# Kernel optimization log

Measured on AMD Instinct MI355X. Metric: run time of the kernel, lower is better.

The kernel has to match this reference:

```python
import jax, jax.numpy as jnp
import numpy as np

N = 100000   # nodes
B = 64       # graphs in batch
E = 1600000  # edges
D_IN = 2
W1D = W2D = W3D = 128
N_CLASSES = 3
MIN_SCORE = 0.1
TOL = 1e-7
BN_EPS = 1e-5


def setup_inputs() -> dict:
    key = jax.random.key(0)
    ks = jax.random.split(key, 32)
    inp = {}
    inp['x'] = jax.random.normal(ks[0], (N, D_IN), jnp.float32)
    inp['edge_index'] = jax.random.randint(ks[1], (2, E), 0, N, dtype=jnp.int32)
    inp['batch_index'] = jnp.sort(jax.random.randint(ks[2], (N,), 0, B, dtype=jnp.int32))
    inp['topk_w'] = jax.random.normal(ks[3], (D_IN,), jnp.float32)
    dims = [(D_IN, W1D), (W1D, W2D), (W2D, W3D)]
    k = 4
    for i, (din, dout) in enumerate(dims, start=1):
        inp[f'W{i}'] = jax.random.normal(ks[k], (din, dout), jnp.float32) * (1.0 / np.sqrt(din)); k += 1
        inp[f'b{i}'] = jax.random.normal(ks[k], (dout,), jnp.float32) * 0.05; k += 1
        inp[f'g{i}'] = 1.0 + 0.1 * jax.random.normal(ks[k], (dout,), jnp.float32); k += 1
        inp[f'be{i}'] = 0.1 * jax.random.normal(ks[k], (dout,), jnp.float32); k += 1
        inp[f'rm{i}'] = 0.1 * jax.random.normal(ks[k], (dout,), jnp.float32); k += 1
        inp[f'rv{i}'] = 1.0 + 0.1 * jax.random.uniform(ks[k], (dout,), jnp.float32); k += 1
    inp['linW'] = jax.random.normal(ks[k], (W3D, N_CLASSES), jnp.float32) * (1.0 / np.sqrt(W3D)); k += 1
    inp['linb'] = jax.random.normal(ks[k], (N_CLASSES,), jnp.float32) * 0.05
    return inp


def _bn_eval(x, g, be, rm, rv):
    # BatchNorm1d in eval mode (running stats)
    return (x - rm) * jax.lax.rsqrt(rv + BN_EPS) * g + be


def _gcn(x, src, dst, ew, W, b):
    # GCNConv: lin -> symmetric-normalized scatter-add (self-loops already in src/dst/ew)
    xw = x @ W                                   # [N, dout]
    deg = jax.ops.segment_sum(ew, dst, num_segments=N)
    dinv = jnp.where(deg > 0, jax.lax.rsqrt(deg), 0.0)
    norm = dinv[src] * ew * dinv[dst]            # [E+N]
    out = jax.ops.segment_sum(norm[:, None] * xw[src], dst, num_segments=N)
    return out + b


def reference(x, edge_index, batch_index, topk_w,
              W1, b1, g1, be1, rm1, rv1,
              W2, b2, g2, be2, rm2, rv2,
              W3, b3, g3, be3, rm3, rv3,
              linW, linb):
    # ---- TopKPooling (min_score mode): per-graph softmax score, threshold keep,
    # x scaled by score. Implemented via masking (fixed shapes): dropped nodes get
    # zero features, zero edge weights, and -inf at the max pool -> math identical
    # to PyG's node filtering (BN is eval-mode, i.e. per-node).
    logits = x @ topk_w                                                    # [N]
    m = jax.ops.segment_max(logits, batch_index, num_segments=B)
    e = jnp.exp(logits - m[batch_index])
    score = e / jax.ops.segment_sum(e, batch_index, num_segments=B)[batch_index]
    smax = jax.ops.segment_max(score, batch_index, num_segments=B)[batch_index] - TOL
    keep = score > jnp.minimum(smax, MIN_SCORE)                            # [N] bool
    keep_f = keep.astype(x.dtype)
    h = x * (score * keep_f)[:, None]

    src0, dst0 = edge_index[0], edge_index[1]
    loop = jnp.arange(N, dtype=src0.dtype)
    src = jnp.concatenate([src0, loop])
    dst = jnp.concatenate([dst0, loop])
    ew = jnp.concatenate([keep_f[src0] * keep_f[dst0], keep_f])            # mask + self-loops

    h = _bn_eval(jax.nn.relu(_gcn(h, src, dst, ew, W1, b1)), g1, be1, rm1, rv1)
    h = _bn_eval(jax.nn.relu(_gcn(h, src, dst, ew, W2, b2)), g2, be2, rm2, rv2)
    h = _bn_eval(jax.nn.relu(_gcn(h, src, dst, ew, W3, b3)), g3, be3, rm3, rv3)

    neg = jnp.finfo(h.dtype).min
    h = jnp.where(keep[:, None], h, neg)
    pooled = jax.ops.segment_max(h, batch_index, num_segments=B)           # [B, w3]
    out = pooled @ linW + linb
    return jax.nn.log_softmax(out, axis=1)
```

## Files before the change

kernel.cpp:

```cpp
#include <hip/hip_runtime.h>

#define NN 100000
#define BB 64
#define EE 1600000
#define FD 128
#define SLOTC 64
#define KSLOTS (BB * SLOTC)
#define EMAXE (1 << 20)
#define NWORDS (NN / 32)
#define STR 391

__device__ __forceinline__ int plower(const int* __restrict__ bidx, int v,
                                      int tid, int* ired) {
    int p = tid * STR;
    int val = bidx[p];
    ired[tid] = (val < v) ? tid : -1;
    __syncthreads();
    for (int s = 128; s > 0; s >>= 1) { if (tid < s) ired[tid] = max(ired[tid], ired[tid + s]); __syncthreads(); }
    int t0 = ired[0];
    __syncthreads();
    if (t0 < 0) return 0;
    int lo = t0 * STR;
    int hi = lo + STR; if (hi > NN) hi = NN;
    int ans = hi;
    for (int q = lo + 1 + tid; q < hi; q += 256) {
        if (bidx[q] >= v) { ans = q; break; }
    }
    ired[tid] = ans;
    __syncthreads();
    for (int s = 128; s > 0; s >>= 1) { if (tid < s) ired[tid] = min(ired[tid], ired[tid + s]); __syncthreads(); }
    int r = ired[0];
    __syncthreads();
    return r;
}

__global__ __launch_bounds__(256) void k_scorekeep(
    const float2* __restrict__ x, const int* __restrict__ bidx,
    const float* __restrict__ tw,
    unsigned* __restrict__ kfbits, int* __restrict__ nslot,
    int* __restrict__ knt, float* __restrict__ degs, float2* __restrict__ h0s,
    int* __restrict__ kecnt)
{
    __shared__ int   ired[256];
    __shared__ float red[256];
    __shared__ int   klist[SLOTC];
    __shared__ int   lcnt;
    __shared__ float shv;
    int b = blockIdx.x, tid = threadIdx.x;
    if (tid == 0) { lcnt = 0; if (b == 0) { kecnt[0] = 0; kecnt[1] = 0; } }
    int s0 = plower(bidx, b, tid, ired);
    int e0 = plower(bidx, b + 1, tid, ired);
    int L = e0 - s0;
    float w0 = tw[0], w1 = tw[1];

    if (L > 0) {
        int wlo = s0 >> 5, whi = (e0 - 1) >> 5;
        for (int w = wlo + tid; w <= whi; w += 256) {
            unsigned mask = 0xFFFFFFFFu;
            if (w == wlo) mask &= (0xFFFFFFFFu << (s0 & 31));
            if (w == whi) mask &= (0xFFFFFFFFu >> (31 - ((e0 - 1) & 31)));
            if (mask == 0xFFFFFFFFu) kfbits[w] = 0u;
            else atomicAnd(&kfbits[w], ~mask);
        }
    }

    float mx = -3.4028235e38f;
    for (int j = tid; j < L; j += 256) {
        float2 v = x[s0 + j];
        mx = fmaxf(mx, v.x * w0 + v.y * w1);
    }
    red[tid] = mx; __syncthreads();
    for (int s = 128; s > 0; s >>= 1) { if (tid < s) red[tid] = fmaxf(red[tid], red[tid + s]); __syncthreads(); }
    if (tid == 0) shv = red[0];
    __syncthreads();
    float m = shv;

    float sm = 0.f;
    for (int j = tid; j < L; j += 256) {
        float2 v = x[s0 + j];
        sm += expf(v.x * w0 + v.y * w1 - m);
    }
    red[tid] = sm; __syncthreads();
    for (int s = 128; s > 0; s >>= 1) { if (tid < s) red[tid] += red[tid + s]; __syncthreads(); }
    if (tid == 0) shv = red[0];
    __syncthreads();
    float S = shv;
    float thr = fminf(1.0f / S - 1e-7f, 0.1f);

    for (int j = tid; j < L; j += 256) {
        float2 v = x[s0 + j];
        float sc = expf(v.x * w0 + v.y * w1 - m) / S;
        if (sc > thr) {
            int l = atomicAdd(&lcnt, 1);
            if (l < SLOTC) klist[l] = j;
        }
    }
    __syncthreads();
    int nk = lcnt; if (nk > SLOTC) nk = SLOTC;
    if (tid == 0) knt[b] = nk;
    for (int l = tid; l < nk; l += 256) {
        int i = s0 + klist[l];
        float2 v = x[i];
        float sc = expf(v.x * w0 + v.y * w1 - m) / S;
        int slot = b * SLOTC + l;
        atomicOr(&kfbits[i >> 5], 1u << (i & 31));
        nslot[i] = slot;
        degs[slot] = 1.0f;
        h0s[slot] = make_float2(v.x * sc, v.y * sc);
    }
}

__global__ void k_edges(const int4* __restrict__ src4, const int* __restrict__ ei,
                        const unsigned* __restrict__ kfbits, const int* __restrict__ nslot,
                        float* __restrict__ degs, int* __restrict__ kedge,
                        int* __restrict__ kecnt) {
    int t = blockIdx.x * 256 + threadIdx.x;
    if (t * 4 >= EE) return;
    int4 s4 = src4[t];
    int ss[4] = {s4.x, s4.y, s4.z, s4.w};
    #pragma unroll
    for (int q = 0; q < 4; q++) {
        int s = ss[q];
        if ((kfbits[s >> 5] >> (s & 31)) & 1u) {
            int d = ei[EE + t * 4 + q];
            if ((kfbits[d >> 5] >> (d & 31)) & 1u) {
                int ds = nslot[d], sl = nslot[s];
                atomicAdd(&degs[ds], 1.0f);
                int idx = atomicAdd(&kecnt[0], 1);
                if (idx < EMAXE) { kedge[2 * idx] = sl; kedge[2 * idx + 1] = ds; }
                if ((sl >> 6) != (ds >> 6)) atomicAdd(&kecnt[1], 1);
            }
        }
    }
}

__global__ __launch_bounds__(256) void k_tail_main(
    const float* __restrict__ degs, const float2* __restrict__ h0s,
    const int* __restrict__ kedge, const int* __restrict__ kecnt,
    const int* __restrict__ knt,
    const float* __restrict__ W1, const float* __restrict__ b1,
    const float* __restrict__ g1, const float* __restrict__ be1,
    const float* __restrict__ rm1, const float* __restrict__ rv1,
    const float* __restrict__ W2, const float* __restrict__ b2,
    const float* __restrict__ g2, const float* __restrict__ be2,
    const float* __restrict__ rm2, const float* __restrict__ rv2,
    const float* __restrict__ W3, const float* __restrict__ b3,
    const float* __restrict__ g3, const float* __restrict__ be3,
    const float* __restrict__ rm3, const float* __restrict__ rv3,
    const float* __restrict__ linW, const float* __restrict__ linb,
    float* __restrict__ hY, float* __restrict__ out)
{
    __shared__ float tileA[SLOTC * FD];
    __shared__ float tileB[SLOTC * FD];
    __shared__ float2 psl[SLOTC];
    __shared__ float poolv[FD];
    __shared__ int keS;
    int b = blockIdx.x, tid = threadIdx.x;
    if (tid == 0) { int k = kecnt[0]; keS = k > EMAXE ? EMAXE : k; }
    for (int j = tid; j < SLOTC; j += 256) psl[j] = make_float2(0.f, 0.f);
    __syncthreads();
    int ke = keS, nk = knt[b], cross = kecnt[1];

    for (int t = tid; t < ke; t += 256) {
        int d = kedge[2 * t + 1];
        if ((d >> 6) == b) {
            int s = kedge[2 * t];
            float nm = rsqrtf(degs[s]) * rsqrtf(degs[d]);
            float2 h = h0s[s];
            atomicAdd(&psl[d & 63].x, nm * h.x);
            atomicAdd(&psl[d & 63].y, nm * h.y);
        }
    }
    __syncthreads();
    for (int j = tid; j < nk * FD; j += 256) {
        int ld = j >> 7, f = j & 127, slot = b * SLOTC + ld;
        float di = rsqrtf(degs[slot]), d2 = di * di;
        float2 h = h0s[slot];
        float a0 = psl[ld].x + d2 * h.x;
        float a1 = psl[ld].y + d2 * h.y;
        float v = a0 * W1[f] + a1 * W1[FD + f] + b1[f];
        v = fmaxf(v, 0.f);
        v = (v - rm1[f]) * rsqrtf(rv1[f] + 1e-5f) * g1[f] + be1[f];
        tileA[j] = v;
    }
    __syncthreads();
    for (int j = tid; j < nk * FD; j += 256) {
        int ld = j >> 7, f = j & 127;
        const float* xr = tileA + ld * FD;
        float acc = 0.f;
        #pragma unroll 8
        for (int k = 0; k < FD; k++) acc += xr[k] * W2[k * FD + f];
        tileB[j] = acc;
    }
    __syncthreads();
    if (cross != 0) {
        for (int j = tid; j < nk * FD; j += 256) {
            int ld = j >> 7, f = j & 127;
            hY[(b * SLOTC + ld) * FD + f] = tileB[j];
        }
        return;
    }
    for (int j = tid; j < nk * FD; j += 256) tileA[j] = 0.f;
    __syncthreads();
    for (long long idx = tid; idx < (long long)ke * FD; idx += 256) {
        int e = (int)(idx >> 7), f = (int)(idx & 127);
        int d = kedge[2 * e + 1];
        if ((d >> 6) == b) {
            int s = kedge[2 * e];
            float nm = rsqrtf(degs[s]) * rsqrtf(degs[d]);
            atomicAdd(&tileA[(d & 63) * FD + f], nm * tileB[(s & 63) * FD + f]);
        }
    }
    __syncthreads();
    for (int j = tid; j < nk * FD; j += 256) {
        int ld = j >> 7, f = j & 127, slot = b * SLOTC + ld;
        float di = rsqrtf(degs[slot]);
        float v = tileA[j] + di * di * tileB[j] + b2[f];
        v = fmaxf(v, 0.f);
        v = (v - rm2[f]) * rsqrtf(rv2[f] + 1e-5f) * g2[f] + be2[f];
        tileA[j] = v;
    }
    __syncthreads();
    for (int j = tid; j < nk * FD; j += 256) {
        int ld = j >> 7, f = j & 127;
        const float* xr = tileA + ld * FD;
        float acc = 0.f;
        #pragma unroll 8
        for (int k = 0; k < FD; k++) acc += xr[k] * W3[k * FD + f];
        tileB[j] = acc;
    }
    __syncthreads();
    for (int j = tid; j < nk * FD; j += 256) tileA[j] = 0.f;
    __syncthreads();
    for (long long idx = tid; idx < (long long)ke * FD; idx += 256) {
        int e = (int)(idx >> 7), f = (int)(idx & 127);
        int d = kedge[2 * e + 1];
        if ((d >> 6) == b) {
            int s = kedge[2 * e];
            float nm = rsqrtf(degs[s]) * rsqrtf(degs[d]);
            atomicAdd(&tileA[(d & 63) * FD + f], nm * tileB[(s & 63) * FD + f]);
        }
    }
    __syncthreads();
    for (int j = tid; j < nk * FD; j += 256) {
        int ld = j >> 7, f = j & 127, slot = b * SLOTC + ld;
        float di = rsqrtf(degs[slot]);
        float v = tileA[j] + di * di * tileB[j] + b3[f];
        v = fmaxf(v, 0.f);
        v = (v - rm3[f]) * rsqrtf(rv3[f] + 1e-5f) * g3[f] + be3[f];
        tileA[j] = v;
    }
    __syncthreads();
    for (int f = tid; f < FD; f += 256) {
        float mx = -3.4028235e38f;
        for (int ld = 0; ld < nk; ld++) mx = fmaxf(mx, tileA[ld * FD + f]);
        poolv[f] = mx;
    }
    __syncthreads();
    if (tid == 0) {
        float z0 = linb[0], z1 = linb[1], z2 = linb[2];
        for (int f = 0; f < FD; f++) {
            float pv = poolv[f];
            z0 += pv * linW[f * 3 + 0];
            z1 += pv * linW[f * 3 + 1];
            z2 += pv * linW[f * 3 + 2];
        }
        float m = fmaxf(z0, fmaxf(z1, z2));
        float l = m + logf(expf(z0 - m) + expf(z1 - m) + expf(z2 - m));
        out[b * 3 + 0] = z0 - l;
        out[b * 3 + 1] = z1 - l;
        out[b * 3 + 2] = z2 - l;
    }
}

__global__ __launch_bounds__(256) void k_tail_slow(
    const float* __restrict__ degs, const int* __restrict__ kedge,
    const int* __restrict__ kecnt, const int* __restrict__ knt,
    const float* __restrict__ hY,
    const float* __restrict__ b2, const float* __restrict__ g2,
    const float* __restrict__ be2, const float* __restrict__ rm2,
    const float* __restrict__ rv2,
    const float* __restrict__ W3, const float* __restrict__ b3,
    const float* __restrict__ g3, const float* __restrict__ be3,
    const float* __restrict__ rm3, const float* __restrict__ rv3,
    const float* __restrict__ linW, const float* __restrict__ linb,
    float* __restrict__ out)
{
    if (kecnt[1] == 0) return;
    __shared__ float tileA[SLOTC * FD];
    __shared__ float tileB[SLOTC * FD];
    __shared__ float rowt[FD];
    __shared__ float poolv[FD];
    __shared__ int keS;
    int b = blockIdx.x, tid = threadIdx.x;
    if (tid == 0) { int k = kecnt[0]; keS = k > EMAXE ? EMAXE : k; }
    __syncthreads();
    int ke = keS, nk = knt[b];

    for (int j = tid; j < nk * FD; j += 256) tileA[j] = 0.f;
    __syncthreads();
    for (long long idx = tid; idx < (long long)ke * FD; idx += 256) {
        int e = (int)(idx >> 7), f = (int)(idx & 127);
        int d = kedge[2 * e + 1];
        if ((d >> 6) == b) {
            int s = kedge[2 * e];
            float nm = rsqrtf(degs[s]) * rsqrtf(degs[d]);
            atomicAdd(&tileA[(d & 63) * FD + f], nm * hY[s * FD + f]);
        }
    }
    __syncthreads();
    for (int j = tid; j < nk * FD; j += 256) {
        int ld = j >> 7, f = j & 127, slot = b * SLOTC + ld;
        float di = rsqrtf(degs[slot]);
        float v = tileA[j] + di * di * hY[slot * FD + f] + b2[f];
        v = fmaxf(v, 0.f);
        v = (v - rm2[f]) * rsqrtf(rv2[f] + 1e-5f) * g2[f] + be2[f];
        tileA[j] = v;
    }
    __syncthreads();
    for (int j = tid; j < nk * FD; j += 256) {
        int ld = j >> 7, f = j & 127;
        const float* xr = tileA + ld * FD;
        float acc = 0.f;
        #pragma unroll 8
        for (int k = 0; k < FD; k++) acc += xr[k] * W3[k * FD + f];
        tileB[j] = acc;
    }
    __syncthreads();
    for (int j = tid; j < nk * FD; j += 256) tileA[j] = 0.f;
    __syncthreads();
    for (long long idx = tid; idx < (long long)ke * FD; idx += 256) {
        int e = (int)(idx >> 7), f = (int)(idx & 127);
        int d = kedge[2 * e + 1];
        if ((d >> 6) == b) {
            int s = kedge[2 * e];
            if ((s >> 6) == b) {
                float nm = rsqrtf(degs[s]) * rsqrtf(degs[d]);
                atomicAdd(&tileA[(d & 63) * FD + f], nm * tileB[(s & 63) * FD + f]);
            }
        }
    }
    __syncthreads();
    for (int e = 0; e < ke; e++) {
        int d = kedge[2 * e + 1];
        if ((d >> 6) != b) continue;
        int s = kedge[2 * e];
        if ((s >> 6) == b) continue;
        float dis = rsqrtf(degs[s]);
        for (int f = tid; f < FD; f += 256) {
            float acc = dis * dis * hY[s * FD + f];
            for (int e2 = 0; e2 < ke; e2++) {
                if (kedge[2 * e2 + 1] == s) {
                    int u = kedge[2 * e2];
                    acc += rsqrtf(degs[u]) * dis * hY[u * FD + f];
                }
            }
            float v = acc + b2[f];
            v = fmaxf(v, 0.f);
            v = (v - rm2[f]) * rsqrtf(rv2[f] + 1e-5f) * g2[f] + be2[f];
            rowt[f] = v;
        }
        __syncthreads();
        float nm = dis * rsqrtf(degs[d]);
        for (int f = tid; f < FD; f += 256) {
            float acc = 0.f;
            #pragma unroll 8
            for (int k = 0; k < FD; k++) acc += rowt[k] * W3[k * FD + f];
            atomicAdd(&tileA[(d & 63) * FD + f], nm * acc);
        }
        __syncthreads();
    }
    for (int j = tid; j < nk * FD; j += 256) {
        int ld = j >> 7, f = j & 127, slot = b * SLOTC + ld;
        float di = rsqrtf(degs[slot]);
        float v = tileA[j] + di * di * tileB[j] + b3[f];
        v = fmaxf(v, 0.f);
        v = (v - rm3[f]) * rsqrtf(rv3[f] + 1e-5f) * g3[f] + be3[f];
        tileA[j] = v;
    }
    __syncthreads();
    for (int f = tid; f < FD; f += 256) {
        float mx = -3.4028235e38f;
        for (int ld = 0; ld < nk; ld++) mx = fmaxf(mx, tileA[ld * FD + f]);
        poolv[f] = mx;
    }
    __syncthreads();
    if (tid == 0) {
        float z0 = linb[0], z1 = linb[1], z2 = linb[2];
        for (int f = 0; f < FD; f++) {
            float pv = poolv[f];
            z0 += pv * linW[f * 3 + 0];
            z1 += pv * linW[f * 3 + 1];
            z2 += pv * linW[f * 3 + 2];
        }
        float m = fmaxf(z0, fmaxf(z1, z2));
        float l = m + logf(expf(z0 - m) + expf(z1 - m) + expf(z2 - m));
        out[b * 3 + 0] = z0 - l;
        out[b * 3 + 1] = z1 - l;
        out[b * 3 + 2] = z2 - l;
    }
}

extern "C" void kernel_launch(void* const* d_in, const int* in_sizes, int n_in,
                              void* d_out, int out_size, void* d_ws, size_t ws_size,
                              hipStream_t stream) {
    (void)in_sizes; (void)n_in; (void)out_size; (void)ws_size;
    const float* x    = (const float*)d_in[0];
    const int*   ei   = (const int*)d_in[1];
    const int*   bidx = (const int*)d_in[2];
    const float* tw   = (const float*)d_in[3];
    const float* W1 = (const float*)d_in[4],  *b1 = (const float*)d_in[5],  *g1 = (const float*)d_in[6];
    const float* be1= (const float*)d_in[7],  *rm1= (const float*)d_in[8],  *rv1= (const float*)d_in[9];
    const float* W2 = (const float*)d_in[10], *b2 = (const float*)d_in[11], *g2 = (const float*)d_in[12];
    const float* be2= (const float*)d_in[13], *rm2= (const float*)d_in[14], *rv2= (const float*)d_in[15];
    const float* W3 = (const float*)d_in[16], *b3 = (const float*)d_in[17], *g3 = (const float*)d_in[18];
    const float* be3= (const float*)d_in[19], *rm3= (const float*)d_in[20], *rv3= (const float*)d_in[21];
    const float* linW = (const float*)d_in[22], *linb = (const float*)d_in[23];
    float* out = (float*)d_out;

    char* w = (char*)d_ws;
    auto take = [&](size_t bytes) { char* r = w; w += (bytes + 255) & ~(size_t)255; return r; };
    int*      kecnt  = (int*)take(16);
    int*      knt    = (int*)take((size_t)BB * 4);
    unsigned* kfbits = (unsigned*)take((size_t)NWORDS * 4);
    int*      nslot  = (int*)take((size_t)NN * 4);
    float*    degs   = (float*)take((size_t)KSLOTS * 4);
    float2*   h0s    = (float2*)take((size_t)KSLOTS * 8);
    int*      kedge  = (int*)take((size_t)EMAXE * 8);
    float*    hY     = (float*)take((size_t)KSLOTS * FD * 4);

    k_scorekeep<<<BB, 256, 0, stream>>>((const float2*)x, bidx, tw,
                                        kfbits, nslot, knt, degs, h0s, kecnt);
    k_edges<<<(EE / 4 + 255) / 256, 256, 0, stream>>>((const int4*)ei, ei, kfbits,
                                                      nslot, degs, kedge, kecnt);
    k_tail_main<<<BB, 256, 0, stream>>>(degs, h0s, kedge, kecnt, knt,
                                        W1, b1, g1, be1, rm1, rv1,
                                        W2, b2, g2, be2, rm2, rv2,
                                        W3, b3, g3, be3, rm3, rv3,
                                        linW, linb, hY, out);
    k_tail_slow<<<BB, 256, 0, stream>>>(degs, kedge, kecnt, knt, hY,
                                        b2, g2, be2, rm2, rv2,
                                        W3, b3, g3, be3, rm3, rv3,
                                        linW, linb, out);
}
```

Before: 143.2 us.

## Fuse edge filtering and GCN tail into one kernel with last-block finisher

Merges the edge-compaction kernel and both tail kernels into a single grid-strided kernel of 512 blocks. A global atomic counter elects the last-finishing block, which then runs all three GCN layers, pooling and the classifier for every graph, using global scratch buffers instead of per-graph shared tiles. This removes two kernel launches and the slow cross-graph fallback path, but all tail work now runs on a single block, which serialises work that was spread across 64 blocks.

```diff
diff --git a/kernel.cpp b/kernel.cpp
--- a/kernel.cpp
+++ b/kernel.cpp
@@ -9,6 +9,7 @@
 #define EMAXE (1 << 20)
 #define NWORDS (NN / 32)
 #define STR 391
+#define GRIDB 512
 
 __device__ __forceinline__ int plower(const int* __restrict__ bidx, int v,
                                       int tid, int* ired) {
@@ -47,7 +48,7 @@
     __shared__ int   lcnt;
     __shared__ float shv;
     int b = blockIdx.x, tid = threadIdx.x;
-    if (tid == 0) { lcnt = 0; if (b == 0) { kecnt[0] = 0; kecnt[1] = 0; } }
+    if (tid == 0) { lcnt = 0; if (b == 0) { kecnt[0] = 0; kecnt[2] = 0; } }
     int s0 = plower(bidx, b, tid, ired);
     int e0 = plower(bidx, b + 1, tid, ired);
     int L = e0 - s0;
@@ -110,34 +111,11 @@
     }
 }
 
-__global__ void k_edges(const int4* __restrict__ src4, const int* __restrict__ ei,
-                        const unsigned* __restrict__ kfbits, const int* __restrict__ nslot,
-                        float* __restrict__ degs, int* __restrict__ kedge,
-                        int* __restrict__ kecnt) {
-    int t = blockIdx.x * 256 + threadIdx.x;
-    if (t * 4 >= EE) return;
-    int4 s4 = src4[t];
-    int ss[4] = {s4.x, s4.y, s4.z, s4.w};
-    #pragma unroll
-    for (int q = 0; q < 4; q++) {
-        int s = ss[q];
-        if ((kfbits[s >> 5] >> (s & 31)) & 1u) {
-            int d = ei[EE + t * 4 + q];
-            if ((kfbits[d >> 5] >> (d & 31)) & 1u) {
-                int ds = nslot[d], sl = nslot[s];
-                atomicAdd(&degs[ds], 1.0f);
-                int idx = atomicAdd(&kecnt[0], 1);
-                if (idx < EMAXE) { kedge[2 * idx] = sl; kedge[2 * idx + 1] = ds; }
-                if ((sl >> 6) != (ds >> 6)) atomicAdd(&kecnt[1], 1);
-            }
-        }
-    }
-}
-
-__global__ __launch_bounds__(256) void k_tail_main(
-    const float* __restrict__ degs, const float2* __restrict__ h0s,
-    const int* __restrict__ kedge, const int* __restrict__ kecnt,
-    const int* __restrict__ knt,
+__global__ __launch_bounds__(256) void k_edge_tail(
+    const int4* __restrict__ src4, const int* __restrict__ ei,
+    const unsigned* __restrict__ kfbits, const int* __restrict__ nslot,
+    float* __restrict__ degs, int* __restrict__ kedge, int* __restrict__ kecnt,
+    const int* __restrict__ knt, const float2* __restrict__ h0s,
     const float* __restrict__ W1, const float* __restrict__ b1,
     const float* __restrict__ g1, const float* __restrict__ be1,
     const float* __restrict__ rm1, const float* __restrict__ rv1,
@@ -148,247 +126,158 @@
     const float* __restrict__ g3, const float* __restrict__ be3,
     const float* __restrict__ rm3, const float* __restrict__ rv3,
     const float* __restrict__ linW, const float* __restrict__ linb,
-    float* __restrict__ hY, float* __restrict__ out)
+    float* __restrict__ hY, float* __restrict__ hAcc,
+    float* __restrict__ out)
 {
-    __shared__ float tileA[SLOTC * FD];
-    __shared__ float tileB[SLOTC * FD];
-    __shared__ float2 psl[SLOTC];
-    __shared__ float poolv[FD];
-    __shared__ int keS;
-    int b = blockIdx.x, tid = threadIdx.x;
-    if (tid == 0) { int k = kecnt[0]; keS = k > EMAXE ? EMAXE : k; }
-    for (int j = tid; j < SLOTC; j += 256) psl[j] = make_float2(0.f, 0.f);
-    __syncthreads();
-    int ke = keS, nk = knt[b], cross = kecnt[1];
-
+    __shared__ float bufA[SLOTC * FD];
+    __shared__ int   rows[KSLOTS];
+    __shared__ int   knt_s[BB];
+    __shared__ int   offs[BB + 1];
+    __shared__ int   lastFlag;
+    int tid = threadIdx.x;
+
+    const int M = EE / 4;
+    for (int t = blockIdx.x * 256 + tid; t < M; t += GRIDB * 256) {
+        int4 s4 = src4[t];
+        int ss[4] = {s4.x, s4.y, s4.z, s4.w};
+        #pragma unroll
+        for (int q = 0; q < 4; q++) {
+            int s = ss[q];
+            if ((kfbits[s >> 5] >> (s & 31)) & 1u) {
+                int d = ei[EE + t * 4 + q];
+                if ((kfbits[d >> 5] >> (d & 31)) & 1u) {
+                    int ds = nslot[d], sl = nslot[s];
+                    atomicAdd(&degs[ds], 1.0f);
+                    int idx = atomicAdd(&kecnt[0], 1);
+                    if (idx < EMAXE) { kedge[2 * idx] = sl; kedge[2 * idx + 1] = ds; }
+                }
+            }
+        }
+    }
+
+    __threadfence();
+    __syncthreads();
+    if (tid == 0) lastFlag = (atomicAdd(&kecnt[2], 1) == GRIDB - 1);
+    __syncthreads();
+    if (!lastFlag) return;
+    __threadfence();
+
+    int ke = kecnt[0]; if (ke > EMAXE) ke = EMAXE;
+
+    if (tid < BB) knt_s[tid] = knt[tid];
+    __syncthreads();
+    if (tid == 0) {
+        int acc = 0;
+        for (int b = 0; b < BB; b++) { offs[b] = acc; acc += knt_s[b]; }
+        offs[BB] = acc;
+    }
+    __syncthreads();
+    int Rtot = offs[BB];
+    for (int b = tid; b < BB; b += 256)
+        for (int l = 0; l < knt_s[b]; l++) rows[offs[b] + l] = b * SLOTC + l;
+    __syncthreads();
+    int RT = Rtot * FD;
+
+    float2* acc2 = (float2*)bufA;
+    for (int r = tid; r < Rtot; r += 256) acc2[rows[r]] = make_float2(0.f, 0.f);
+    __syncthreads();
     for (int t = tid; t < ke; t += 256) {
-        int d = kedge[2 * t + 1];
-        if ((d >> 6) == b) {
-            int s = kedge[2 * t];
-            float nm = rsqrtf(degs[s]) * rsqrtf(degs[d]);
-            float2 h = h0s[s];
-            atomicAdd(&psl[d & 63].x, nm * h.x);
-            atomicAdd(&psl[d & 63].y, nm * h.y);
-        }
-    }
-    __syncthreads();
-    for (int j = tid; j < nk * FD; j += 256) {
-        int ld = j >> 7, f = j & 127, slot = b * SLOTC + ld;
+        int s = kedge[2 * t], d = kedge[2 * t + 1];
+        float nm = rsqrtf(degs[s]) * rsqrtf(degs[d]);
+        float2 h = h0s[s];
+        atomicAdd(&acc2[d].x, nm * h.x);
+        atomicAdd(&acc2[d].y, nm * h.y);
+    }
+    __syncthreads();
+
+    for (int j = tid; j < RT; j += 256) {
+        int r = j >> 7, f = j & 127, slot = rows[r];
         float di = rsqrtf(degs[slot]), d2 = di * di;
         float2 h = h0s[slot];
-        float a0 = psl[ld].x + d2 * h.x;
-        float a1 = psl[ld].y + d2 * h.y;
+        float a0 = acc2[slot].x + d2 * h.x;
+        float a1 = acc2[slot].y + d2 * h.y;
         float v = a0 * W1[f] + a1 * W1[FD + f] + b1[f];
         v = fmaxf(v, 0.f);
         v = (v - rm1[f]) * rsqrtf(rv1[f] + 1e-5f) * g1[f] + be1[f];
-        tileA[j] = v;
-    }
-    __syncthreads();
-    for (int j = tid; j < nk * FD; j += 256) {
-        int ld = j >> 7, f = j & 127;
-        const float* xr = tileA + ld * FD;
+        hAcc[slot * FD + f] = v;
+    }
+    __syncthreads();
+
+    for (int j = tid; j < RT; j += 256) {
+        int r = j >> 7, f = j & 127, slot = rows[r];
+        const float* xr = hAcc + slot * FD;
         float acc = 0.f;
         #pragma unroll 8
         for (int k = 0; k < FD; k++) acc += xr[k] * W2[k * FD + f];
-        tileB[j] = acc;
-    }
-    __syncthreads();
-    if (cross != 0) {
-        for (int j = tid; j < nk * FD; j += 256) {
-            int ld = j >> 7, f = j & 127;
-            hY[(b * SLOTC + ld) * FD + f] = tileB[j];
-        }
-        return;
-    }
-    for (int j = tid; j < nk * FD; j += 256) tileA[j] = 0.f;
+        hY[slot * FD + f] = acc;
+    }
+    __syncthreads();
+
+    for (int j = tid; j < RT; j += 256) hAcc[rows[j >> 7] * FD + (j & 127)] = 0.f;
     __syncthreads();
     for (long long idx = tid; idx < (long long)ke * FD; idx += 256) {
         int e = (int)(idx >> 7), f = (int)(idx & 127);
-        int d = kedge[2 * e + 1];
-        if ((d >> 6) == b) {
-            int s = kedge[2 * e];
-            float nm = rsqrtf(degs[s]) * rsqrtf(degs[d]);
-            atomicAdd(&tileA[(d & 63) * FD + f], nm * tileB[(s & 63) * FD + f]);
-        }
-    }
-    __syncthreads();
-    for (int j = tid; j < nk * FD; j += 256) {
-        int ld = j >> 7, f = j & 127, slot = b * SLOTC + ld;
+        int s = kedge[2 * e], d = kedge[2 * e + 1];
+        float nm = rsqrtf(degs[s]) * rsqrtf(degs[d]);
+        atomicAdd(&hAcc[d * FD + f], nm * hY[s * FD + f]);
+    }
+    __syncthreads();
+
+    for (int j = tid; j < RT; j += 256) {
+        int r = j >> 7, f = j & 127, slot = rows[r];
         float di = rsqrtf(degs[slot]);
-        float v = tileA[j] + di * di * tileB[j] + b2[f];
+        float v = hAcc[slot * FD + f] + di * di * hY[slot * FD + f] + b2[f];
         v = fmaxf(v, 0.f);
         v = (v - rm2[f]) * rsqrtf(rv2[f] + 1e-5f) * g2[f] + be2[f];
-        tileA[j] = v;
-    }
-    __syncthreads();
-    for (int j = tid; j < nk * FD; j += 256) {
-        int ld = j >> 7, f = j & 127;
-        const float* xr = tileA + ld * FD;
+        hAcc[slot * FD + f] = v;
+    }
+    __syncthreads();
+
+    for (int j = tid; j < RT; j += 256) {
+        int r = j >> 7, f = j & 127, slot = rows[r];
+        const float* xr = hAcc + slot * FD;
         float acc = 0.f;
         #pragma unroll 8
         for (int k = 0; k < FD; k++) acc += xr[k] * W3[k * FD + f];
-        tileB[j] = acc;
-    }
-    __syncthreads();
-    for (int j = tid; j < nk * FD; j += 256) tileA[j] = 0.f;
+        hY[slot * FD + f] = acc;
+    }
+    __syncthreads();
+
+    for (int j = tid; j < RT; j += 256) hAcc[rows[j >> 7] * FD + (j & 127)] = 0.f;
     __syncthreads();
     for (long long idx = tid; idx < (long long)ke * FD; idx += 256) {
         int e = (int)(idx >> 7), f = (int)(idx & 127);
-        int d = kedge[2 * e + 1];
-        if ((d >> 6) == b) {
-            int s = kedge[2 * e];
-            float nm = rsqrtf(degs[s]) * rsqrtf(degs[d]);
-            atomicAdd(&tileA[(d & 63) * FD + f], nm * tileB[(s & 63) * FD + f]);
-        }
-    }
-    __syncthreads();
-    for (int j = tid; j < nk * FD; j += 256) {
-        int ld = j >> 7, f = j & 127, slot = b * SLOTC + ld;
+        int s = kedge[2 * e], d = kedge[2 * e + 1];
+        float nm = rsqrtf(degs[s]) * rsqrtf(degs[d]);
+        atomicAdd(&hAcc[d * FD + f], nm * hY[s * FD + f]);
+    }
+    __syncthreads();
+
+    for (int j = tid; j < RT; j += 256) {
+        int r = j >> 7, f = j & 127, slot = rows[r];
         float di = rsqrtf(degs[slot]);
-        float v = tileA[j] + di * di * tileB[j] + b3[f];
+        float v = hAcc[slot * FD + f] + di * di * hY[slot * FD + f] + b3[f];
         v = fmaxf(v, 0.f);
         v = (v - rm3[f]) * rsqrtf(rv3[f] + 1e-5f) * g3[f] + be3[f];
-        tileA[j] = v;
-    }
-    __syncthreads();
-    for (int f = tid; f < FD; f += 256) {
+        hAcc[slot * FD + f] = v;
+    }
+    __syncthreads();
+
+    float* pool = bufA;
+    for (int j = tid; j < BB * FD; j += 256) {
+        int b = j >> 7, f = j & 127;
         float mx = -3.4028235e38f;
-        for (int ld = 0; ld < nk; ld++) mx = fmaxf(mx, tileA[ld * FD + f]);
-        poolv[f] = mx;
-    }
-    __syncthreads();
-    if (tid == 0) {
+        int nk = knt_s[b];
+        for (int l = 0; l < nk; l++) mx = fmaxf(mx, hAcc[(b * SLOTC + l) * FD + f]);
+        pool[j] = mx;
+    }
+    __syncthreads();
+
+    if (tid < BB) {
+        int b = tid;
         float z0 = linb[0], z1 = linb[1], z2 = linb[2];
         for (int f = 0; f < FD; f++) {
-            float pv = poolv[f];
-            z0 += pv * linW[f * 3 + 0];
-            z1 += pv * linW[f * 3 + 1];
-            z2 += pv * linW[f * 3 + 2];
-        }
-        float m = fmaxf(z0, fmaxf(z1, z2));
-        float l = m + logf(expf(z0 - m) + expf(z1 - m) + expf(z2 - m));
-        out[b * 3 + 0] = z0 - l;
-        out[b * 3 + 1] = z1 - l;
-        out[b * 3 + 2] = z2 - l;
-    }
-}
-
-__global__ __launch_bounds__(256) void k_tail_slow(
-    const float* __restrict__ degs, const int* __restrict__ kedge,
-    const int* __restrict__ kecnt, const int* __restrict__ knt,
-    const float* __restrict__ hY,
-    const float* __restrict__ b2, const float* __restrict__ g2,
-    const float* __restrict__ be2, const float* __restrict__ rm2,
-    const float* __restrict__ rv2,
-    const float* __restrict__ W3, const float* __restrict__ b3,
-    const float* __restrict__ g3, const float* __restrict__ be3,
-    const float* __restrict__ rm3, const float* __restrict__ rv3,
-    const float* __restrict__ linW, const float* __restrict__ linb,
-    float* __restrict__ out)
-{
-    if (kecnt[1] == 0) return;
-    __shared__ float tileA[SLOTC * FD];
-    __shared__ float tileB[SLOTC * FD];
-    __shared__ float rowt[FD];
-    __shared__ float poolv[FD];
-    __shared__ int keS;
-    int b = blockIdx.x, tid = threadIdx.x;
-    if (tid == 0) { int k = kecnt[0]; keS = k > EMAXE ? EMAXE : k; }
-    __syncthreads();
-    int ke = keS, nk = knt[b];
-
-    for (int j = tid; j < nk * FD; j += 256) tileA[j] = 0.f;
-    __syncthreads();
-    for (long long idx = tid; idx < (long long)ke * FD; idx += 256) {
-        int e = (int)(idx >> 7), f = (int)(idx & 127);
-        int d = kedge[2 * e + 1];
-        if ((d >> 6) == b) {
-            int s = kedge[2 * e];
-            float nm = rsqrtf(degs[s]) * rsqrtf(degs[d]);
-            atomicAdd(&tileA[(d & 63) * FD + f], nm * hY[s * FD + f]);
-        }
-    }
-    __syncthreads();
-    for (int j = tid; j < nk * FD; j += 256) {
-        int ld = j >> 7, f = j & 127, slot = b * SLOTC + ld;
-        float di = rsqrtf(degs[slot]);
-        float v = tileA[j] + di * di * hY[slot * FD + f] + b2[f];
-        v = fmaxf(v, 0.f);
-        v = (v - rm2[f]) * rsqrtf(rv2[f] + 1e-5f) * g2[f] + be2[f];
-        tileA[j] = v;
-    }
-    __syncthreads();
-    for (int j = tid; j < nk * FD; j += 256) {
-        int ld = j >> 7, f = j & 127;
-        const float* xr = tileA + ld * FD;
-        float acc = 0.f;
-        #pragma unroll 8
-        for (int k = 0; k < FD; k++) acc += xr[k] * W3[k * FD + f];
-        tileB[j] = acc;
-    }
-    __syncthreads();
-    for (int j = tid; j < nk * FD; j += 256) tileA[j] = 0.f;
-    __syncthreads();
-    for (long long idx = tid; idx < (long long)ke * FD; idx += 256) {
-        int e = (int)(idx >> 7), f = (int)(idx & 127);
-        int d = kedge[2 * e + 1];
-        if ((d >> 6) == b) {
-            int s = kedge[2 * e];
-            if ((s >> 6) == b) {
-                float nm = rsqrtf(degs[s]) * rsqrtf(degs[d]);
-                atomicAdd(&tileA[(d & 63) * FD + f], nm * tileB[(s & 63) * FD + f]);
-            }
-        }
-    }
-    __syncthreads();
-    for (int e = 0; e < ke; e++) {
-        int d = kedge[2 * e + 1];
-        if ((d >> 6) != b) continue;
-        int s = kedge[2 * e];
-        if ((s >> 6) == b) continue;
-        float dis = rsqrtf(degs[s]);
-        for (int f = tid; f < FD; f += 256) {
-            float acc = dis * dis * hY[s * FD + f];
-            for (int e2 = 0; e2 < ke; e2++) {
-                if (kedge[2 * e2 + 1] == s) {
-                    int u = kedge[2 * e2];
-                    acc += rsqrtf(degs[u]) * dis * hY[u * FD + f];
-                }
-            }
-            float v = acc + b2[f];
-            v = fmaxf(v, 0.f);
-            v = (v - rm2[f]) * rsqrtf(rv2[f] + 1e-5f) * g2[f] + be2[f];
-            rowt[f] = v;
-        }
-        __syncthreads();
-        float nm = dis * rsqrtf(degs[d]);
-        for (int f = tid; f < FD; f += 256) {
-            float acc = 0.f;
-            #pragma unroll 8
-            for (int k = 0; k < FD; k++) acc += rowt[k] * W3[k * FD + f];
-            atomicAdd(&tileA[(d & 63) * FD + f], nm * acc);
-        }
-        __syncthreads();
-    }
-    for (int j = tid; j < nk * FD; j += 256) {
-        int ld = j >> 7, f = j & 127, slot = b * SLOTC + ld;
-        float di = rsqrtf(degs[slot]);
-        float v = tileA[j] + di * di * tileB[j] + b3[f];
-        v = fmaxf(v, 0.f);
-        v = (v - rm3[f]) * rsqrtf(rv3[f] + 1e-5f) * g3[f] + be3[f];
-        tileA[j] = v;
-    }
-    __syncthreads();
-    for (int f = tid; f < FD; f += 256) {
-        float mx = -3.4028235e38f;
-        for (int ld = 0; ld < nk; ld++) mx = fmaxf(mx, tileA[ld * FD + f]);
-        poolv[f] = mx;
-    }
-    __syncthreads();
-    if (tid == 0) {
-        float z0 = linb[0], z1 = linb[1], z2 = linb[2];
-        for (int f = 0; f < FD; f++) {
-            float pv = poolv[f];
+            float pv = pool[b * FD + f];
             z0 += pv * linW[f * 3 + 0];
             z1 += pv * linW[f * 3 + 1];
             z2 += pv * linW[f * 3 + 2];
@@ -428,18 +317,14 @@
     float2*   h0s    = (float2*)take((size_t)KSLOTS * 8);
     int*      kedge  = (int*)take((size_t)EMAXE * 8);
     float*    hY     = (float*)take((size_t)KSLOTS * FD * 4);
+    float*    hAcc   = (float*)take((size_t)KSLOTS * FD * 4);
 
     k_scorekeep<<<BB, 256, 0, stream>>>((const float2*)x, bidx, tw,
                                         kfbits, nslot, knt, degs, h0s, kecnt);
-    k_edges<<<(EE / 4 + 255) / 256, 256, 0, stream>>>((const int4*)ei, ei, kfbits,
-                                                      nslot, degs, kedge, kecnt);
-    k_tail_main<<<BB, 256, 0, stream>>>(degs, h0s, kedge, kecnt, knt,
-                                        W1, b1, g1, be1, rm1, rv1,
-                                        W2, b2, g2, be2, rm2, rv2,
-                                        W3, b3, g3, be3, rm3, rv3,
-                                        linW, linb, hY, out);
-    k_tail_slow<<<BB, 256, 0, stream>>>(degs, kedge, kecnt, knt, hY,
-                                        b2, g2, be2, rm2, rv2,
-                                        W3, b3, g3, be3, rm3, rv3,
-                                        linW, linb, out);
+    k_edge_tail<<<GRIDB, 256, 0, stream>>>((const int4*)ei, ei, kfbits, nslot,
+                                           degs, kedge, kecnt, knt, h0s,
+                                           W1, b1, g1, be1, rm1, rv1,
+                                           W2, b2, g2, be2, rm2, rv2,
+                                           W3, b3, g3, be3, rm3, rv3,
+                                           linW, linb, hY, hAcc, out);
 }
```

After: 362.1 us. 153% more time.

## Merge tail kernels into one and recompute cross-graph rows locally

Applied to the files above, without the earlier changes.

Combines the main and slow tail kernels into a single kernel and removes the global hY buffer. When edges cross graph slots, the rows each block needs are recomputed on the fly from layer-1 inputs instead of being exchanged through global memory. The common no-cross path is unchanged apart from the second kernel launch that is no longer made. The cross path can become very expensive because it rescans the edge list per row, and it adds a third 32KB shared tile, which raises LDS use per block.

```diff
diff --git a/kernel.cpp b/kernel.cpp
--- a/kernel.cpp
+++ b/kernel.cpp
@@ -134,7 +134,7 @@
     }
 }
 
-__global__ __launch_bounds__(256) void k_tail_main(
+__global__ __launch_bounds__(256) void k_tail(
     const float* __restrict__ degs, const float2* __restrict__ h0s,
     const int* __restrict__ kedge, const int* __restrict__ kecnt,
     const int* __restrict__ knt,
@@ -148,12 +148,19 @@
     const float* __restrict__ g3, const float* __restrict__ be3,
     const float* __restrict__ rm3, const float* __restrict__ rv3,
     const float* __restrict__ linW, const float* __restrict__ linb,
-    float* __restrict__ hY, float* __restrict__ out)
+    float* __restrict__ out)
 {
     __shared__ float tileA[SLOTC * FD];
     __shared__ float tileB[SLOTC * FD];
+    __shared__ float tileC[SLOTC * FD];
     __shared__ float2 psl[SLOTC];
     __shared__ float poolv[FD];
+    __shared__ float rowT[FD];
+    __shared__ float rowY[FD];
+    __shared__ float rowAgg[FD];
+    __shared__ float rowH2[FD];
+    __shared__ float rowB[FD];
+    __shared__ float2 aggs;
     __shared__ int keS;
     int b = blockIdx.x, tid = threadIdx.x;
     if (tid == 0) { int k = kecnt[0]; keS = k > EMAXE ? EMAXE : k; }
@@ -193,25 +200,154 @@
         tileB[j] = acc;
     }
     __syncthreads();
-    if (cross != 0) {
+
+    if (cross == 0) {
+        for (int j = tid; j < nk * FD; j += 256) tileA[j] = 0.f;
+        __syncthreads();
+        for (long long idx = tid; idx < (long long)ke * FD; idx += 256) {
+            int e = (int)(idx >> 7), f = (int)(idx & 127);
+            int d = kedge[2 * e + 1];
+            if ((d >> 6) == b) {
+                int s = kedge[2 * e];
+                float nm = rsqrtf(degs[s]) * rsqrtf(degs[d]);
+                atomicAdd(&tileA[(d & 63) * FD + f], nm * tileB[(s & 63) * FD + f]);
+            }
+        }
+        __syncthreads();
+        for (int j = tid; j < nk * FD; j += 256) {
+            int ld = j >> 7, f = j & 127, slot = b * SLOTC + ld;
+            float di = rsqrtf(degs[slot]);
+            float v = tileA[j] + di * di * tileB[j] + b2[f];
+            v = fmaxf(v, 0.f);
+            v = (v - rm2[f]) * rsqrtf(rv2[f] + 1e-5f) * g2[f] + be2[f];
+            tileA[j] = v;
+        }
+        __syncthreads();
         for (int j = tid; j < nk * FD; j += 256) {
             int ld = j >> 7, f = j & 127;
-            hY[(b * SLOTC + ld) * FD + f] = tileB[j];
+            const float* xr = tileA + ld * FD;
+            float acc = 0.f;
+            #pragma unroll 8
+            for (int k = 0; k < FD; k++) acc += xr[k] * W3[k * FD + f];
+            tileB[j] = acc;
+        }
+        __syncthreads();
+        for (int j = tid; j < nk * FD; j += 256) tileA[j] = 0.f;
+        __syncthreads();
+        for (long long idx = tid; idx < (long long)ke * FD; idx += 256) {
+            int e = (int)(idx >> 7), f = (int)(idx & 127);
+            int d = kedge[2 * e + 1];
+            if ((d >> 6) == b) {
+                int s = kedge[2 * e];
+                float nm = rsqrtf(degs[s]) * rsqrtf(degs[d]);
+                atomicAdd(&tileA[(d & 63) * FD + f], nm * tileB[(s & 63) * FD + f]);
+            }
+        }
+        __syncthreads();
+        for (int j = tid; j < nk * FD; j += 256) {
+            int ld = j >> 7, f = j & 127, slot = b * SLOTC + ld;
+            float di = rsqrtf(degs[slot]);
+            float v = tileA[j] + di * di * tileB[j] + b3[f];
+            v = fmaxf(v, 0.f);
+            v = (v - rm3[f]) * rsqrtf(rv3[f] + 1e-5f) * g3[f] + be3[f];
+            tileA[j] = v;
+        }
+        __syncthreads();
+        for (int f = tid; f < FD; f += 256) {
+            float mx = -3.4028235e38f;
+            for (int ld = 0; ld < nk; ld++) mx = fmaxf(mx, tileA[ld * FD + f]);
+            poolv[f] = mx;
+        }
+        __syncthreads();
+        if (tid == 0) {
+            float z0 = linb[0], z1 = linb[1], z2 = linb[2];
+            for (int f = 0; f < FD; f++) {
+                float pv = poolv[f];
+                z0 += pv * linW[f * 3 + 0];
+                z1 += pv * linW[f * 3 + 1];
+                z2 += pv * linW[f * 3 + 2];
+            }
+            float m = fmaxf(z0, fmaxf(z1, z2));
+            float l = m + logf(expf(z0 - m) + expf(z1 - m) + expf(z2 - m));
+            out[b * 3 + 0] = z0 - l;
+            out[b * 3 + 1] = z1 - l;
+            out[b * 3 + 2] = z2 - l;
         }
         return;
     }
+
+    auto hY_row = [&](int s) {
+        if (tid == 0) aggs = make_float2(0.f, 0.f);
+        __syncthreads();
+        float a0 = 0.f, a1 = 0.f;
+        for (int e = tid; e < ke; e += 256) {
+            if (kedge[2 * e + 1] == s) {
+                int u = kedge[2 * e];
+                float nm = rsqrtf(degs[u]) * rsqrtf(degs[s]);
+                float2 h = h0s[u];
+                a0 += nm * h.x; a1 += nm * h.y;
+            }
+        }
+        atomicAdd(&aggs.x, a0); atomicAdd(&aggs.y, a1);
+        __syncthreads();
+        float di = rsqrtf(degs[s]), d2 = di * di;
+        float2 h = h0s[s];
+        float A0 = aggs.x + d2 * h.x, A1 = aggs.y + d2 * h.y;
+        for (int f = tid; f < FD; f += 256) {
+            float v = A0 * W1[f] + A1 * W1[FD + f] + b1[f];
+            v = fmaxf(v, 0.f);
+            v = (v - rm1[f]) * rsqrtf(rv1[f] + 1e-5f) * g1[f] + be1[f];
+            rowT[f] = v;
+        }
+        __syncthreads();
+        for (int f = tid; f < FD; f += 256) {
+            float acc = 0.f;
+            for (int k = 0; k < FD; k++) acc += rowT[k] * W2[k * FD + f];
+            rowY[f] = acc;
+        }
+        __syncthreads();
+    };
+    auto hYB_row = [&](int s) {
+        for (int f = tid; f < FD; f += 256) rowAgg[f] = 0.f;
+        __syncthreads();
+        for (int e = 0; e < ke; e++) {
+            if (kedge[2 * e + 1] != s) continue;
+            int u = kedge[2 * e];
+            hY_row(u);
+            float nm = rsqrtf(degs[u]) * rsqrtf(degs[s]);
+            for (int f = tid; f < FD; f += 256) rowAgg[f] += nm * rowY[f];
+            __syncthreads();
+        }
+        hY_row(s);
+        float di = rsqrtf(degs[s]);
+        for (int f = tid; f < FD; f += 256) {
+            float v = rowAgg[f] + di * di * rowY[f] + b2[f];
+            v = fmaxf(v, 0.f);
+            v = (v - rm2[f]) * rsqrtf(rv2[f] + 1e-5f) * g2[f] + be2[f];
+            rowH2[f] = v;
+        }
+        __syncthreads();
+        for (int f = tid; f < FD; f += 256) {
+            float acc = 0.f;
+            for (int k = 0; k < FD; k++) acc += rowH2[k] * W3[k * FD + f];
+            rowB[f] = acc;
+        }
+        __syncthreads();
+    };
+
     for (int j = tid; j < nk * FD; j += 256) tileA[j] = 0.f;
     __syncthreads();
-    for (long long idx = tid; idx < (long long)ke * FD; idx += 256) {
-        int e = (int)(idx >> 7), f = (int)(idx & 127);
+    for (int e = 0; e < ke; e++) {
         int d = kedge[2 * e + 1];
-        if ((d >> 6) == b) {
-            int s = kedge[2 * e];
-            float nm = rsqrtf(degs[s]) * rsqrtf(degs[d]);
-            atomicAdd(&tileA[(d & 63) * FD + f], nm * tileB[(s & 63) * FD + f]);
-        }
-    }
-    __syncthreads();
+        if ((d >> 6) != b) continue;
+        int s = kedge[2 * e];
+        float nm = rsqrtf(degs[s]) * rsqrtf(degs[d]);
+        const float* srow;
+        if ((s >> 6) == b) srow = &tileB[(s & 63) * FD];
+        else { hY_row(s); srow = rowY; }
+        for (int f = tid; f < FD; f += 256) tileA[(d & 63) * FD + f] += nm * srow[f];
+        __syncthreads();
+    }
     for (int j = tid; j < nk * FD; j += 256) {
         int ld = j >> 7, f = j & 127, slot = b * SLOTC + ld;
         float di = rsqrtf(degs[slot]);
@@ -227,153 +363,28 @@
         float acc = 0.f;
         #pragma unroll 8
         for (int k = 0; k < FD; k++) acc += xr[k] * W3[k * FD + f];
-        tileB[j] = acc;
-    }
-    __syncthreads();
-    for (int j = tid; j < nk * FD; j += 256) tileA[j] = 0.f;
-    __syncthreads();
-    for (long long idx = tid; idx < (long long)ke * FD; idx += 256) {
-        int e = (int)(idx >> 7), f = (int)(idx & 127);
-        int d = kedge[2 * e + 1];
-        if ((d >> 6) == b) {
-            int s = kedge[2 * e];
-            float nm = rsqrtf(degs[s]) * rsqrtf(degs[d]);
-            atomicAdd(&tileA[(d & 63) * FD + f], nm * tileB[(s & 63) * FD + f]);
-        }
-    }
-    __syncthreads();
-    for (int j = tid; j < nk * FD; j += 256) {
-        int ld = j >> 7, f = j & 127, slot = b * SLOTC + ld;
-        float di = rsqrtf(degs[slot]);
-        float v = tileA[j] + di * di * tileB[j] + b3[f];
-        v = fmaxf(v, 0.f);
-        v = (v - rm3[f]) * rsqrtf(rv3[f] + 1e-5f) * g3[f] + be3[f];
-        tileA[j] = v;
-    }
-    __syncthreads();
-    for (int f = tid; f < FD; f += 256) {
-        float mx = -3.4028235e38f;
-        for (int ld = 0; ld < nk; ld++) mx = fmaxf(mx, tileA[ld * FD + f]);
-        poolv[f] = mx;
-    }
-    __syncthreads();
-    if (tid == 0) {
-        float z0 = linb[0], z1 = linb[1], z2 = linb[2];
-        for (int f = 0; f < FD; f++) {
-            float pv = poolv[f];
-            z0 += pv * linW[f * 3 + 0];
-            z1 += pv * linW[f * 3 + 1];
-            z2 += pv * linW[f * 3 + 2];
-        }
-        float m = fmaxf(z0, fmaxf(z1, z2));
-        float l = m + logf(expf(z0 - m) + expf(z1 - m) + expf(z2 - m));
-        out[b * 3 + 0] = z0 - l;
-        out[b * 3 + 1] = z1 - l;
-        out[b * 3 + 2] = z2 - l;
-    }
-}
-
-__global__ __launch_bounds__(256) void k_tail_slow(
-    const float* __restrict__ degs, const int* __restrict__ kedge,
-    const int* __restrict__ kecnt, const int* __restrict__ knt,
-    const float* __restrict__ hY,
-    const float* __restrict__ b2, const float* __restrict__ g2,
-    const float* __restrict__ be2, const float* __restrict__ rm2,
-    const float* __restrict__ rv2,
-    const float* __restrict__ W3, const float* __restrict__ b3,
-    const float* __restrict__ g3, const float* __restrict__ be3,
-    const float* __restrict__ rm3, const float* __restrict__ rv3,
-    const float* __restrict__ linW, const float* __restrict__ linb,
-    float* __restrict__ out)
-{
-    if (kecnt[1] == 0) return;
-    __shared__ float tileA[SLOTC * FD];
-    __shared__ float tileB[SLOTC * FD];
-    __shared__ float rowt[FD];
-    __shared__ float poolv[FD];
-    __shared__ int keS;
-    int b = blockIdx.x, tid = threadIdx.x;
-    if (tid == 0) { int k = kecnt[0]; keS = k > EMAXE ? EMAXE : k; }
-    __syncthreads();
-    int ke = keS, nk = knt[b];
-
-    for (int j = tid; j < nk * FD; j += 256) tileA[j] = 0.f;
-    __syncthreads();
-    for (long long idx = tid; idx < (long long)ke * FD; idx += 256) {
-        int e = (int)(idx >> 7), f = (int)(idx & 127);
-        int d = kedge[2 * e + 1];
-        if ((d >> 6) == b) {
-            int s = kedge[2 * e];
-            float nm = rsqrtf(degs[s]) * rsqrtf(degs[d]);
-            atomicAdd(&tileA[(d & 63) * FD + f], nm * hY[s * FD + f]);
-        }
-    }
-    __syncthreads();
-    for (int j = tid; j < nk * FD; j += 256) {
-        int ld = j >> 7, f = j & 127, slot = b * SLOTC + ld;
-        float di = rsqrtf(degs[slot]);
-        float v = tileA[j] + di * di * hY[slot * FD + f] + b2[f];
-        v = fmaxf(v, 0.f);
-        v = (v - rm2[f]) * rsqrtf(rv2[f] + 1e-5f) * g2[f] + be2[f];
-        tileA[j] = v;
-    }
-    __syncthreads();
-    for (int j = tid; j < nk * FD; j += 256) {
-        int ld = j >> 7, f = j & 127;
-        const float* xr = tileA + ld * FD;
-        float acc = 0.f;
-        #pragma unroll 8
-        for (int k = 0; k < FD; k++) acc += xr[k] * W3[k * FD + f];
-        tileB[j] = acc;
-    }
-    __syncthreads();
-    for (int j = tid; j < nk * FD; j += 256) tileA[j] = 0.f;
-    __syncthreads();
-    for (long long idx = tid; idx < (long long)ke * FD; idx += 256) {
-        int e = (int)(idx >> 7), f = (int)(idx & 127);
-        int d = kedge[2 * e + 1];
-        if ((d >> 6) == b) {
-            int s = kedge[2 * e];
-            if ((s >> 6) == b) {
-                float nm = rsqrtf(degs[s]) * rsqrtf(degs[d]);
-                atomicAdd(&tileA[(d & 63) * FD + f], nm * tileB[(s & 63) * FD + f]);
-            }
-        }
-    }
+        tileC[j] = acc;
+    }
+    __syncthreads();
+    for (int j = tid; j < nk * FD; j += 256) tileB[j] = tileC[j];
+    __syncthreads();
+    for (int j = tid; j < nk * FD; j += 256) tileC[j] = 0.f;
     __syncthreads();
     for (int e = 0; e < ke; e++) {
         int d = kedge[2 * e + 1];
         if ((d >> 6) != b) continue;
         int s = kedge[2 * e];
-        if ((s >> 6) == b) continue;
-        float dis = rsqrtf(degs[s]);
-        for (int f = tid; f < FD; f += 256) {
-            float acc = dis * dis * hY[s * FD + f];
-            for (int e2 = 0; e2 < ke; e2++) {
-                if (kedge[2 * e2 + 1] == s) {
-                    int u = kedge[2 * e2];
-                    acc += rsqrtf(degs[u]) * dis * hY[u * FD + f];
-                }
-            }
-            float v = acc + b2[f];
-            v = fmaxf(v, 0.f);
-            v = (v - rm2[f]) * rsqrtf(rv2[f] + 1e-5f) * g2[f] + be2[f];
-            rowt[f] = v;
-        }
-        __syncthreads();
-        float nm = dis * rsqrtf(degs[d]);
-        for (int f = tid; f < FD; f += 256) {
-            float acc = 0.f;
-            #pragma unroll 8
-            for (int k = 0; k < FD; k++) acc += rowt[k] * W3[k * FD + f];
-            atomicAdd(&tileA[(d & 63) * FD + f], nm * acc);
-        }
+        float nm = rsqrtf(degs[s]) * rsqrtf(degs[d]);
+        const float* srow;
+        if ((s >> 6) == b) srow = &tileB[(s & 63) * FD];
+        else { hYB_row(s); srow = rowB; }
+        for (int f = tid; f < FD; f += 256) tileC[(d & 63) * FD + f] += nm * srow[f];
         __syncthreads();
     }
     for (int j = tid; j < nk * FD; j += 256) {
         int ld = j >> 7, f = j & 127, slot = b * SLOTC + ld;
         float di = rsqrtf(degs[slot]);
-        float v = tileA[j] + di * di * tileB[j] + b3[f];
+        float v = tileC[j] + di * di * tileB[j] + b3[f];
         v = fmaxf(v, 0.f);
         v = (v - rm3[f]) * rsqrtf(rv3[f] + 1e-5f) * g3[f] + be3[f];
         tileA[j] = v;
@@ -427,19 +438,14 @@
     float*    degs   = (float*)take((size_t)KSLOTS * 4);
     float2*   h0s    = (float2*)take((size_t)KSLOTS * 8);
     int*      kedge  = (int*)take((size_t)EMAXE * 8);
-    float*    hY     = (float*)take((size_t)KSLOTS * FD * 4);
 
     k_scorekeep<<<BB, 256, 0, stream>>>((const float2*)x, bidx, tw,
                                         kfbits, nslot, knt, degs, h0s, kecnt);
     k_edges<<<(EE / 4 + 255) / 256, 256, 0, stream>>>((const int4*)ei, ei, kfbits,
                                                       nslot, degs, kedge, kecnt);
-    k_tail_main<<<BB, 256, 0, stream>>>(degs, h0s, kedge, kecnt, knt,
-                                        W1, b1, g1, be1, rm1, rv1,
-                                        W2, b2, g2, be2, rm2, rv2,
-                                        W3, b3, g3, be3, rm3, rv3,
-                                        linW, linb, hY, out);
-    k_tail_slow<<<BB, 256, 0, stream>>>(degs, kedge, kecnt, knt, hY,
-                                        b2, g2, be2, rm2, rv2,
-                                        W3, b3, g3, be3, rm3, rv3,
-                                        linW, linb, out);
+    k_tail<<<BB, 256, 0, stream>>>(degs, h0s, kedge, kecnt, knt,
+                                   W1, b1, g1, be1, rm1, rv1,
+                                   W2, b2, g2, be2, rm2, rv2,
+                                   W3, b3, g3, be3, rm3, rv3,
+                                   linW, linb, out);
 }
```

Measured after the change: 149.1 us. 4.1% more time.
